# Optimization experiments

Measured on AMD Instinct MI355X. Metric: run time of the kernel, lower is better.

Reference implementation:

```python
import jax, jax.numpy as jnp
import numpy as np

# Atom/task routing tables (from module constants)
ATOM = {'vm': 0, 'im': 1, 'cm': 2, 'sc': 3, 'cc': 4}
TASK_PAIRS = [('vm', 'sc'), ('vm', 'cc'), ('im', 'sc'), ('im', 'cc'), ('cm', 'sc'), ('cm', 'cc')]
SRC_IDX = np.array([[ATOM[l], ATOM[r]] for l, r in TASK_PAIRS], dtype=np.int32)  # [6,2]
DST_IDX = np.array([[ATOM[r], ATOM[l]] for l, r in TASK_PAIRS], dtype=np.int32)  # [6,2]
NCLS = 6
NATOMS = 5


def _l2norm(x, eps=1e-12):
    return x / jnp.clip(jnp.linalg.norm(x, axis=-1, keepdims=True), eps)


def setup_inputs() -> dict:
    key = jax.random.key(0)
    ks = jax.random.split(key, 12)
    B, NPATCH, D, H = 64, 197, 768, 3072
    std = 0.02
    x = jax.random.normal(ks[0], (B, NCLS + NPATCH, D), dtype=jnp.float32)
    fc1_w = jax.random.normal(ks[1], (H, D), dtype=jnp.float32) * std
    fc1_b = jnp.zeros((H,), jnp.float32)
    fc2_w = jax.random.normal(ks[2], (D, H), dtype=jnp.float32) * std
    fc2_b = jnp.zeros((D,), jnp.float32)
    gate_pair = jax.random.normal(ks[3], (NCLS, 2, D), dtype=jnp.float32) * std
    atom_in_w = jax.random.normal(ks[4], (NATOMS, H, D), dtype=jnp.float32) * std
    atom_in_b = jax.random.normal(ks[5], (NATOMS, H), dtype=jnp.float32) * std
    atom_out_w = jax.random.normal(ks[6], (NATOMS, D, H), dtype=jnp.float32) * std
    atom_out_b = jax.random.normal(ks[7], (NATOMS, D), dtype=jnp.float32) * std
    balance_bias = jnp.zeros((NCLS, 2), jnp.float32)
    return {'x': x, 'fc1_w': fc1_w, 'fc1_b': fc1_b, 'fc2_w': fc2_w, 'fc2_b': fc2_b,
            'gate_pair': gate_pair, 'atom_in_w': atom_in_w, 'atom_in_b': atom_in_b,
            'atom_out_w': atom_out_w, 'atom_out_b': atom_out_b, 'balance_bias': balance_bias}


def reference(x, fc1_w, fc1_b, fc2_w, fc2_b, gate_pair, atom_in_w, atom_in_b,
              atom_out_w, atom_out_b, balance_bias):
    src = jnp.asarray(SRC_IDX)
    dst = jnp.asarray(DST_IDX)
    D = x.shape[-1]
    H = atom_in_w.shape[1]
    cls_tokens = x[:, :NCLS]          # [B, ncls, D]
    patch_tokens = x[:, NCLS:]        # [B, Np, D]

    # Plain patch MLP (fc1 -> GELU -> fc2); dropout p=0.03 is identity at eval.
    patch_out = jax.nn.gelu(patch_tokens @ fc1_w.T + fc1_b, approximate=False) @ fc2_w.T + fc2_b

    # Pair-wise gate logits on L2-normalized inputs/weights (float32 math).
    gate_in = _l2norm(cls_tokens.astype(jnp.float32))
    gate_w = _l2norm(gate_pair.astype(jnp.float32))
    gate_logits = jnp.einsum('bnd,nrd->bnr', gate_in, gate_w) + balance_bias[None]
    route_probs = jax.nn.softmax(gate_logits, axis=-1)        # [B, ncls, 2]
    chosen_route = jnp.argmax(route_probs, axis=-1)           # [B, ncls]

    # All-atom input projections + GELU: [B, ncls, natoms, H]
    hid_all = jax.nn.gelu(jnp.einsum('bnd,ahd->bnah', cls_tokens, atom_in_w)
                          + atom_in_b[None, None], approximate=False)
    # Gather the source atom per (task, route): [B, ncls, 2, H]
    sh_pair = hid_all[:, jnp.arange(NCLS)[:, None], src, :]
    # Destination expert output weights: [ncls, 2, D, H]
    route_out_w = atom_out_w[dst.reshape(-1)].reshape(NCLS, 2, D, H)
    route_candidates = jnp.einsum('bnrh,nrdh->bnrd', sh_pair, route_out_w) + atom_out_b[dst][None]

    # Hard argmax dispatch, weighted by the chosen route probability.
    chosen_w = jnp.take_along_axis(route_probs, chosen_route[..., None], axis=-1)  # [B, ncls, 1]
    chosen_cand = jnp.take_along_axis(route_candidates, chosen_route[:, :, None, None], axis=2)[:, :, 0]
    cls_out = chosen_cand * chosen_w.astype(chosen_cand.dtype)

    return jnp.concatenate([cls_out, patch_out], axis=1)
```

## Files before the change

kernel.cpp:

```cpp
#include <hip/hip_runtime.h>
#include <hip/hip_bf16.h>


typedef __bf16 bf16x8 __attribute__((ext_vector_type(8)));
typedef float f32x4 __attribute__((ext_vector_type(4)));
typedef unsigned short u16;

#define DEVINL __device__ __forceinline__

DEVINL u16 f2bf(float f) {
  __bf16 h = (__bf16)f;
  return __builtin_bit_cast(u16, h);
}

DEVINL float gelu_fast(float v) {
  const float x2 = 0.5f * v * v;
  const float t = x2 * (1.27323954f + 0.147f * x2) / (1.0f + 0.147f * x2);
  const float r = sqrtf(fmaxf(1.0f - __expf(-t), 0.0f));
  const float e = copysignf(r, v);
  return 0.5f * v * (1.0f + e);
}

DEVINL void async_load16(const void* g, void* l) {
  __builtin_amdgcn_global_load_lds(
      (const __attribute__((address_space(1))) unsigned int*)g,
      (__attribute__((address_space(3))) unsigned int*)l, 16, 0, 0);
}

#define MFMA16 __builtin_amdgcn_mfma_f32_16x16x32_bf16

__global__ void cvt_gate(const float* __restrict__ x, u16* __restrict__ xc, u16* __restrict__ xp,
                         const float* __restrict__ s1, u16* __restrict__ d1,
                         const float* __restrict__ s2, u16* __restrict__ d2,
                         const float* __restrict__ s3, u16* __restrict__ d3,
                         const float* __restrict__ s4, u16* __restrict__ d4,
                         const float* __restrict__ gate_pair,
                         const float* __restrict__ balance_bias,
                         int* __restrict__ rstar, float* __restrict__ wstar) {
  int b = blockIdx.x;
  if (b < 9744) {
    const int e = (b * 256 + threadIdx.x) * 4;
    const int t = e / 768, dd = e % 768;
    const int bb = t / 203, i = t % 203;
    const float4 v = *(const float4*)(x + e);
    ushort4 u;
    u.x = f2bf(v.x); u.y = f2bf(v.y); u.z = f2bf(v.z); u.w = f2bf(v.w);
    if (i < 6) *(ushort4*)(xc + (size_t)(bb * 6 + i) * 768 + dd) = u;
    else       *(ushort4*)(xp + (size_t)(bb * 197 + (i - 6)) * 768 + dd) = u;
    return;
  }
  b -= 9744;
  if (b < 27648) {
    const float* s; u16* d;
    if (b < 2304) { s = s1; d = d1; }
    else if (b < 4608) { s = s2; d = d2; b -= 2304; }
    else if (b < 16128) { s = s3; d = d3; b -= 4608; }
    else { s = s4; d = d4; b -= 16128; }
    const int i = (b * 256 + threadIdx.x) * 4;
    const float4 v = *(const float4*)(s + i);
    ushort4 u;
    u.x = f2bf(v.x); u.y = f2bf(v.y); u.z = f2bf(v.z); u.w = f2bf(v.w);
    *(ushort4*)(d + i) = u;
    return;
  }
  b -= 27648;
  const int lane = threadIdx.x & 63, wid = threadIdx.x >> 6;
  const int idx = b * 4 + wid;
  const int bb = idx / 6, n = idx % 6;
  const float* xv = x + (size_t)(bb * 203 + n) * 768;
  const float* w0 = gate_pair + (size_t)(n * 2 + 0) * 768;
  const float* w1 = gate_pair + (size_t)(n * 2 + 1) * 768;
  double xx = 0, a00 = 0, a11 = 0, p0 = 0, p1 = 0;
  for (int d = lane; d < 768; d += 64) {
    double xd = xv[d], g0 = w0[d], g1 = w1[d];
    xx += xd * xd; a00 += g0 * g0; a11 += g1 * g1; p0 += xd * g0; p1 += xd * g1;
  }
#pragma unroll
  for (int off = 32; off; off >>= 1) {
    xx  += __shfl_xor(xx, off);
    a00 += __shfl_xor(a00, off);
    a11 += __shfl_xor(a11, off);
    p0  += __shfl_xor(p0, off);
    p1  += __shfl_xor(p1, off);
  }
  if (lane == 0) {
    double nx = fmax(sqrt(xx), 1e-12), n0 = fmax(sqrt(a00), 1e-12), n1 = fmax(sqrt(a11), 1e-12);
    double l0 = p0 / (nx * n0) + (double)balance_bias[n * 2 + 0];
    double l1 = p1 / (nx * n1) + (double)balance_bias[n * 2 + 1];
    const int r = (l1 > l0) ? 1 : 0;
    double m = fmax(l0, l1);
    double e0 = exp(l0 - m), e1 = exp(l1 - m);
    rstar[idx] = r;
    wstar[idx] = (float)(((r == 1) ? e1 : e0) / (e0 + e1));
  }
}

template <int EPI>
DEVINL void gemm_body(const u16* __restrict__ A, const u16* __restrict__ B,
                      const float* __restrict__ bias, void* __restrict__ Cout,
                      int M, int K, int ldc, int bx, int by, u16* As, u16* Bs) {
  const int tid = threadIdx.x;
  const int lane = tid & 63, wid = tid >> 6;
  const int wr = wid >> 1, wc = wid & 1;
  const int tm = by * 128, tn = bx * 128;
  const int rA = lane >> 3, sA = lane & 7;
  const int ksteps = K >> 6;

  f32x4 acc[4][4] = {};

  for (int ks = 0; ks < ksteps; ++ks) {
    const int k0 = ks << 6;
#pragma unroll
    for (int c = 0; c < 4; ++c) {
      const int chunk = wid * 4 + c;
      const int row   = chunk * 8 + rA;
      int grow = tm + row;
      grow = grow < M ? grow : (M - 1);
      const int slot = sA ^ (row & 7);
      async_load16(A + (size_t)grow * K + k0 + slot * 8, (char*)As + chunk * 1024);
    }
#pragma unroll
    for (int c = 0; c < 4; ++c) {
      const int chunk = wid * 4 + c;
      const int row   = chunk * 8 + rA;
      const int slot  = sA ^ (row & 7);
      async_load16(B + (size_t)(tn + row) * K + k0 + slot * 8, (char*)Bs + chunk * 1024);
    }
    __syncthreads();
#pragma unroll
    for (int kk = 0; kk < 2; ++kk) {
      bf16x8 af[4], bfv[4];
#pragma unroll
      for (int im = 0; im < 4; ++im) {
        const int R = wr * 64 + im * 16 + (lane & 15);
        const int s = (kk * 4 + (lane >> 4)) ^ (R & 7);
        af[im] = *(const bf16x8*)((const char*)As + R * 128 + s * 16);
      }
#pragma unroll
      for (int in_ = 0; in_ < 4; ++in_) {
        const int R = wc * 64 + in_ * 16 + (lane & 15);
        const int s = (kk * 4 + (lane >> 4)) ^ (R & 7);
        bfv[in_] = *(const bf16x8*)((const char*)Bs + R * 128 + s * 16);
      }
#pragma unroll
      for (int im = 0; im < 4; ++im)
#pragma unroll
        for (int in_ = 0; in_ < 4; ++in_)
          acc[im][in_] = MFMA16(af[im], bfv[in_], acc[im][in_], 0, 0, 0);
    }
    __syncthreads();
  }

  const int cn = lane & 15, cr4 = (lane >> 4) * 4;
  const int col0 = tn + wc * 64 + cn;
  const int r0 = tm + wr * 64;
  int b197 = 0, p197 = 0;
  if (EPI == 1) { b197 = r0 / 197; p197 = r0 % 197; }
#pragma unroll
  for (int im = 0; im < 4; ++im) {
#pragma unroll
    for (int in_ = 0; in_ < 4; ++in_) {
      const int col = col0 + in_ * 16;
      const float bv = bias[col];
#pragma unroll
      for (int j = 0; j < 4; ++j) {
        const int off = im * 16 + cr4 + j;
        const int row = r0 + off;
        if (row < M) {
          const float v = acc[im][in_][j] + bv;
          if (EPI == 0) {
            ((u16*)Cout)[(size_t)row * ldc + col] = f2bf(gelu_fast(v));
          } else {
            int pp = p197 + off, bb = b197;
            if (pp >= 197) { pp -= 197; ++bb; }
            ((float*)Cout)[((size_t)(bb * 203 + 6 + pp)) * 768 + col] = v;
          }
        }
      }
    }
  }
}

DEVINL void cand_body(const u16* __restrict__ hid, const u16* __restrict__ wao,
                      const float* __restrict__ bout, const int* __restrict__ rstar,
                      const float* __restrict__ wstar, float* __restrict__ out,
                      int bx, int g, int bz, char* smem) {
  const int n = g >> 1, r = g & 1;
  const int src_a = (r == 0) ? (n >> 1) : (3 + (n & 1));
  const int dst_a = (r == 1) ? (n >> 1) : (3 + (n & 1));
  const int tn = bx * 128;
  const int b0 = bz * 32;
  const int tid = threadIdx.x, lane = tid & 63, wid = tid >> 6;
  const u16* Bbase = wao + (size_t)dst_a * 768 * 3072;
  const u16* Abase = hid + (size_t)src_a * 3072 + (size_t)n * 15360;

  f32x4 acc[2][2] = {};

  auto stage = [&](int buf, int t) {
    const int k0 = t << 6;
    {
      const int row = tid >> 3;
      const int slA = (tid & 7) ^ (row & 7);
      async_load16(Abase + (size_t)(b0 + row) * 6 * 15360 + k0 + slA * 8,
                   smem + buf * 4096 + row * 128 + (tid & 7) * 16);
    }
#pragma unroll
    for (int j = 0; j < 4; ++j) {
      const int row = j * 32 + (tid >> 3);
      const int slB = (tid & 7) ^ (row & 7);
      async_load16(Bbase + (size_t)(tn + row) * 3072 + k0 + slB * 8,
                   smem + 8192 + buf * 16384 + row * 128 + (tid & 7) * 16);
    }
  };
  auto compute = [&](int buf) {
    const u16* as = (const u16*)(smem + buf * 4096);
    const u16* bs = (const u16*)(smem + 8192 + buf * 16384);
#pragma unroll
    for (int kk = 0; kk < 2; ++kk) {
      bf16x8 af[2], bfv[2];
#pragma unroll
      for (int im = 0; im < 2; ++im) {
        const int R = im * 16 + (lane & 15);
        const int s = (kk * 4 + (lane >> 4)) ^ (R & 7);
        af[im] = *(const bf16x8*)(as + R * 64 + s * 8);
      }
#pragma unroll
      for (int q = 0; q < 2; ++q) {
        const int R = wid * 32 + q * 16 + (lane & 15);
        const int s = (kk * 4 + (lane >> 4)) ^ (R & 7);
        bfv[q] = *(const bf16x8*)(bs + R * 64 + s * 8);
      }
#pragma unroll
      for (int im = 0; im < 2; ++im)
#pragma unroll
        for (int q = 0; q < 2; ++q)
          acc[im][q] = MFMA16(af[im], bfv[q], acc[im][q], 0, 0, 0);
    }
  };

  stage(0, 0);
  __syncthreads();
  for (int t = 0; t < 48; ++t) {
    if (t + 1 < 48) stage((t + 1) & 1, t + 1);
    compute(t & 1);
    __syncthreads();
  }

  const int cn = lane & 15, cr4 = (lane >> 4) * 4;
#pragma unroll
  for (int im = 0; im < 2; ++im)
#pragma unroll
    for (int q = 0; q < 2; ++q) {
      const int col = tn + wid * 32 + q * 16 + cn;
      const float bv = bout[dst_a * 768 + col];
#pragma unroll
      for (int j = 0; j < 4; ++j) {
        const int b = b0 + im * 16 + cr4 + j;
        const int idx = b * 6 + n;
        if (rstar[idx] == r)
          out[((size_t)(b * 203 + n)) * 768 + col] = (acc[im][q][j] + bv) * wstar[idx];
      }
    }
}

__global__ __launch_bounds__(256, 2) void gemm_f1(
    const u16* __restrict__ xp, const u16* __restrict__ w1, const float* __restrict__ fc1b,
    u16* __restrict__ hb,
    const u16* __restrict__ xc, const u16* __restrict__ wai, const float* __restrict__ aib,
    u16* __restrict__ hidb) {
  __shared__ u16 As[128 * 64];
  __shared__ u16 Bs[128 * 64];
  int id = blockIdx.x;
  if (id < 2376) {
    id = (id & 7) * 297 + (id >> 3);
    gemm_body<0>(xp, w1, fc1b, hb, 12608, 768, 3072, id % 24, id / 24, As, Bs);
  } else {
    id -= 2376;
    gemm_body<0>(xc, wai, aib, hidb, 384, 768, 15360, id % 120, id / 120, As, Bs);
  }
}

__global__ __launch_bounds__(256, 2) void gemm_f2(
    const u16* __restrict__ hb, const u16* __restrict__ w2, const float* __restrict__ fc2b,
    float* __restrict__ out,
    const u16* __restrict__ hidb, const u16* __restrict__ wao, const float* __restrict__ aob,
    const int* __restrict__ rstar, const float* __restrict__ wstar) {
  __shared__ char smem[40960];
  int id = blockIdx.x;
  if (id < 594) {
    const int xcd = id & 7, k = id >> 3;
    id = (xcd < 2 ? xcd * 75 : 150 + (xcd - 2) * 74) + k;
    gemm_body<1>(hb, w2, fc2b, out, 12608, 3072, 768, id % 6, id / 6,
                 (u16*)smem, (u16*)(smem + 16384));
  } else {
    id -= 594;
    cand_body(hidb, wao, aob, rstar, wstar, out, id % 6, (id / 6) % 12, id / 72, smem);
  }
}

extern "C" void kernel_launch(void* const* d_in, const int* in_sizes, int n_in,
                              void* d_out, int out_size, void* d_ws, size_t ws_size,
                              hipStream_t stream) {
  const float* x     = (const float*)d_in[0];
  const float* fc1w  = (const float*)d_in[1];
  const float* fc1b  = (const float*)d_in[2];
  const float* fc2w  = (const float*)d_in[3];
  const float* fc2b  = (const float*)d_in[4];
  const float* gpair = (const float*)d_in[5];
  const float* aiw   = (const float*)d_in[6];
  const float* aib   = (const float*)d_in[7];
  const float* aow   = (const float*)d_in[8];
  const float* aob   = (const float*)d_in[9];
  const float* bbias = (const float*)d_in[10];
  float* out = (float*)d_out;

  char* ws = (char*)d_ws;
  u16* xp   = (u16*)(ws + 0);
  u16* xc   = (u16*)(ws + 19365888);
  u16* w1   = (u16*)(ws + 19955712);
  u16* w2   = (u16*)(ws + 24674304);
  u16* wai  = (u16*)(ws + 29392896);
  u16* wao  = (u16*)(ws + 52985856);
  u16* hb   = (u16*)(ws + 76578816);
  u16* hid  = (u16*)(ws + 154042368);
  int*   rstar = (int*)(ws + 165838848);
  float* wstar = (float*)(ws + 165840384);
  if (ws_size < 165841920) return;

  cvt_gate<<<37488, 256, 0, stream>>>(x, xc, xp, fc1w, w1, fc2w, w2, aiw, wai, aow, wao,
                                      gpair, bbias, rstar, wstar);
  gemm_f1<<<2736, 256, 0, stream>>>(xp, w1, fc1b, hb, xc, wai, aib, hid);
  gemm_f2<<<738, 256, 0, stream>>>(hb, w2, fc2b, out, hid, wao, aob, rstar, wstar);
}
```

Measured before the change: 234.3 us.

## Move fc2 and atom-out weight conversion into the fc1 GEMM launch

The fp32-to-bf16 conversion of the fc2 and atom_out weights moves out of the first conversion kernel and into trailing blocks of the fc1 GEMM launch. Those blocks can fill the GPU while the GEMM tiles drain, and the first kernel gets shorter. The XCD-aware block remapping for the fc1 GEMM is also removed, which may hurt L2 locality. Because the 13824 conversion blocks come last in the grid, they may simply run after the GEMM blocks rather than overlapping with them.

Result: no change. 231.7 us, median of 2 (-1.1%).

```diff
diff --git a/kernel.cpp b/kernel.cpp
--- a/kernel.cpp
+++ b/kernel.cpp
@@ -30,10 +30,8 @@
 #define MFMA16 __builtin_amdgcn_mfma_f32_16x16x32_bf16
 
 __global__ void cvt_gate(const float* __restrict__ x, u16* __restrict__ xc, u16* __restrict__ xp,
-                         const float* __restrict__ s1, u16* __restrict__ d1,
-                         const float* __restrict__ s2, u16* __restrict__ d2,
-                         const float* __restrict__ s3, u16* __restrict__ d3,
-                         const float* __restrict__ s4, u16* __restrict__ d4,
+                         const float* __restrict__ fc1w, u16* __restrict__ w1,
+                         const float* __restrict__ aiw, u16* __restrict__ wai,
                          const float* __restrict__ gate_pair,
                          const float* __restrict__ balance_bias,
                          int* __restrict__ rstar, float* __restrict__ wstar) {
@@ -50,12 +48,10 @@
     return;
   }
   b -= 9744;
-  if (b < 27648) {
+  if (b < 13824) {
     const float* s; u16* d;
-    if (b < 2304) { s = s1; d = d1; }
-    else if (b < 4608) { s = s2; d = d2; b -= 2304; }
-    else if (b < 16128) { s = s3; d = d3; b -= 4608; }
-    else { s = s4; d = d4; b -= 16128; }
+    if (b < 2304) { s = fc1w; d = w1; }
+    else { s = aiw; d = wai; b -= 2304; }
     const int i = (b * 256 + threadIdx.x) * 4;
     const float4 v = *(const float4*)(s + i);
     ushort4 u;
@@ -63,16 +59,16 @@
     *(ushort4*)(d + i) = u;
     return;
   }
-  b -= 27648;
+  b -= 13824;
   const int lane = threadIdx.x & 63, wid = threadIdx.x >> 6;
   const int idx = b * 4 + wid;
   const int bb = idx / 6, n = idx % 6;
   const float* xv = x + (size_t)(bb * 203 + n) * 768;
   const float* w0 = gate_pair + (size_t)(n * 2 + 0) * 768;
-  const float* w1 = gate_pair + (size_t)(n * 2 + 1) * 768;
+  const float* w1g = gate_pair + (size_t)(n * 2 + 1) * 768;
   double xx = 0, a00 = 0, a11 = 0, p0 = 0, p1 = 0;
   for (int d = lane; d < 768; d += 64) {
-    double xd = xv[d], g0 = w0[d], g1 = w1[d];
+    double xd = xv[d], g0 = w0[d], g1 = w1g[d];
     xx += xd * xd; a00 += g0 * g0; a11 += g1 * g1; p0 += xd * g0; p1 += xd * g1;
   }
 #pragma unroll
@@ -267,16 +263,27 @@
     const u16* __restrict__ xp, const u16* __restrict__ w1, const float* __restrict__ fc1b,
     u16* __restrict__ hb,
     const u16* __restrict__ xc, const u16* __restrict__ wai, const float* __restrict__ aib,
-    u16* __restrict__ hidb) {
+    u16* __restrict__ hidb,
+    const float* __restrict__ fc2w, u16* __restrict__ w2,
+    const float* __restrict__ aow, u16* __restrict__ wao) {
   __shared__ u16 As[128 * 64];
   __shared__ u16 Bs[128 * 64];
   int id = blockIdx.x;
   if (id < 2376) {
-    id = (id & 7) * 297 + (id >> 3);
     gemm_body<0>(xp, w1, fc1b, hb, 12608, 768, 3072, id % 24, id / 24, As, Bs);
-  } else {
+  } else if (id < 2736) {
     id -= 2376;
     gemm_body<0>(xc, wai, aib, hidb, 384, 768, 15360, id % 120, id / 120, As, Bs);
+  } else {
+    id -= 2736;
+    const float* s; u16* d;
+    if (id < 2304) { s = fc2w; d = w2; }
+    else { s = aow; d = wao; id -= 2304; }
+    const int i = (id * 256 + threadIdx.x) * 4;
+    const float4 v = *(const float4*)(s + i);
+    ushort4 u;
+    u.x = f2bf(v.x); u.y = f2bf(v.y); u.z = f2bf(v.z); u.w = f2bf(v.w);
+    *(ushort4*)(d + i) = u;
   }
 }
 
@@ -327,8 +334,9 @@
   float* wstar = (float*)(ws + 165840384);
   if (ws_size < 165841920) return;
 
-  cvt_gate<<<37488, 256, 0, stream>>>(x, xc, xp, fc1w, w1, fc2w, w2, aiw, wai, aow, wao,
+  cvt_gate<<<23664, 256, 0, stream>>>(x, xc, xp, fc1w, w1, aiw, wai,
                                       gpair, bbias, rstar, wstar);
-  gemm_f1<<<2736, 256, 0, stream>>>(xp, w1, fc1b, hb, xc, wai, aib, hid);
+  gemm_f1<<<16560, 256, 0, stream>>>(xp, w1, fc1b, hb, xc, wai, aib, hid,
+                                     fc2w, w2, aow, wao);
   gemm_f2<<<738, 256, 0, stream>>>(hb, w2, fc2b, out, hid, wao, aob, rstar, wstar);
 }
```
